# Kernel tuning notes

Hardware: AMD Instinct MI355X
Metric: run time of the kernel (lower is better)

## Reference

```python
import jax, jax.numpy as jnp
import numpy as np


def _prelu(x, a):
    # torch.nn.PReLU with per-channel parameter a (broadcast over batch)
    return jnp.where(x >= 0, x, a * x)


def setup_inputs() -> dict:
    key = jax.random.key(0)
    ks = jax.random.split(key, 12)
    B = 8192
    dims = [512, 1024, 1024, 512]  # tardim
    E = 8                          # tctrl = modim[-1]
    scale = 0.02                   # keep activations well-scaled across 3 layers
    inp = {
        "x": jax.random.normal(ks[0], (B, dims[0]), dtype=jnp.float32),
        "weights": jax.random.uniform(ks[1], (E,), dtype=jnp.float32),
    }
    for i in range(3):
        din, dout = dims[i], dims[i + 1]
        inp[f"W{i}"] = jax.random.normal(ks[2 + 3 * i], (E, din, dout), dtype=jnp.float32) * scale
        inp[f"b{i}"] = jax.random.normal(ks[3 + 3 * i], (E, dout), dtype=jnp.float32) * scale
        inp[f"a{i}"] = jnp.full((dout,), 0.25, dtype=jnp.float32)  # PReLU init
    return inp


def reference(x, weights, W0, b0, a0, W1, b1, a1, W2, b2, a2):
    # mie.g: per layer, weighted sum over tctrl expert Linears, then PReLU.
    # sum_j (w_j/sum(w)) * (x @ W_j + b_j) == x @ (sum_j wn_j W_j) + sum_j wn_j b_j,
    # so pre-merge expert weights (tiny contraction) and do one GEMM per layer.
    wn = weights / jnp.sum(weights)  # [E]
    for W, b, a in ((W0, b0, a0), (W1, b1, a1), (W2, b2, a2)):
        Wm = jnp.einsum('e,eio->io', wn, W)  # merged weight [in, out]
        bm = jnp.einsum('e,eo->o', wn, b)    # merged bias   [out]
        x = _prelu(x @ Wm + bm, a)           # [B, out]
    return x
```

## Files before the change

kernel.cpp:

```cpp
#include <hip/hip_runtime.h>
#include <stdint.h>

typedef unsigned short u16;
typedef __attribute__((ext_vector_type(8))) short short8;
typedef __attribute__((ext_vector_type(4))) float float4v;

__device__ __forceinline__ u16 f2bf(float f) {
    union { float f; uint32_t u; } v; v.f = f;
    uint32_t r = v.u + 0x7fffu + ((v.u >> 16) & 1u);
    return (u16)(r >> 16);
}

__device__ __forceinline__ void gload16(const u16* g, u16* l) {
    __builtin_amdgcn_global_load_lds(
        (const __attribute__((address_space(1))) void*)g,
        (__attribute__((address_space(3))) void*)l, 16, 0, 0);
}

__device__ __forceinline__ float load_wn(const float* wts, float* wn) {
    float s = 0.f;
    #pragma unroll
    for (int e = 0; e < 8; ++e) { wn[e] = wts[e]; s += wn[e]; }
    return 1.0f / s;
}

__device__ __forceinline__ void merge_tile(
    const float* __restrict__ W, u16* __restrict__ Wt, int K, int N, int lb,
    const float* wn, float inv, float (*tile)[33], int tid) {
    const int ntiles = N >> 5;
    const int o0 = (lb % ntiles) * 32, i0 = (lb / ntiles) * 32;
    const int tx = tid & 31, ty = tid >> 5;
    #pragma unroll
    for (int s4 = 0; s4 < 4; ++s4) {
        int il = ty + s4 * 8;
        float acc = 0.f;
        #pragma unroll
        for (int e = 0; e < 8; ++e)
            acc += wn[e] * W[(size_t)e * K * N + (size_t)(i0 + il) * N + o0 + tx];
        tile[il][tx] = acc * inv;
    }
    __syncthreads();
    #pragma unroll
    for (int s4 = 0; s4 < 4; ++s4) {
        int ol = ty + s4 * 8;
        Wt[(size_t)(o0 + ol) * K + i0 + tx] = f2bf(tile[tx][ol]);
    }
}

__global__ __launch_bounds__(256) void prep_fused(
    const float* __restrict__ x, u16* __restrict__ xbf,
    const float* __restrict__ wts,
    const float* __restrict__ W0, u16* __restrict__ W0t,
    const float* __restrict__ b0, const float* __restrict__ b1, const float* __restrict__ b2,
    float* __restrict__ bm) {
    __shared__ float tile[32][33];
    const int b = blockIdx.x, tid = threadIdx.x;

    if (b < 4096) {
        int i = (b * 256 + tid) * 4;
        float4 v = *(const float4*)(x + i);
        union { u16 s[4]; uint64_t q; } o;
        o.s[0] = f2bf(v.x); o.s[1] = f2bf(v.y); o.s[2] = f2bf(v.z); o.s[3] = f2bf(v.w);
        *(uint64_t*)(xbf + i) = o.q;
        return;
    }

    float wn[8]; const float inv = load_wn(wts, wn);

    if (b < 4608) {
        merge_tile(W0, W0t, 512, 1024, b - 4096, wn, inv, tile, tid);
        return;
    }

    int t = (b - 4608) * 256 + tid;
    if (t >= 2560) return;
    const float* bp; int o, stride;
    if (t < 1024)      { bp = b0; o = t;        stride = 1024; }
    else if (t < 2048) { bp = b1; o = t - 1024; stride = 1024; }
    else               { bp = b2; o = t - 2048; stride = 512;  }
    float acc = 0.f;
    #pragma unroll
    for (int e = 0; e < 8; ++e) acc += wn[e] * bp[e * stride + o];
    bm[t] = acc * inv;
}

template <int BN, bool OUT_F32, bool MERGE>
__global__ __launch_bounds__(256, 2) void gemm_bias_prelu(
    const u16* __restrict__ A, const u16* __restrict__ Bt,
    const float* __restrict__ bias, const float* __restrict__ alpha,
    void* __restrict__ outp, int M, int N, int K,
    const float* __restrict__ wts, const float* __restrict__ Wm,
    u16* __restrict__ Wmt, int K2, int N2) {
    __shared__ __align__(16) u16 sh[(128 + BN) * 64];
    const int tid = threadIdx.x;
    const int nbn = N / BN;
    const int nGemm = nbn * (M >> 7);
    const int bid = blockIdx.x;

    if (MERGE && bid >= nGemm) {
        float wn[8]; const float inv = load_wn(wts, wn);
        merge_tile(Wm, Wmt, K2, N2, bid - nGemm, wn, inv, (float(*)[33])(void*)sh, tid);
        return;
    }

    const int bn = bid % nbn, bm = bid / nbn;
    u16* As = sh;
    u16* Bs = sh + 128 * 64;

    const int r0 = tid >> 3;
    const int p  = tid & 7;
    const int c  = p ^ (r0 & 7);
    const u16* Ag = A  + (size_t)(bm * 128 + r0) * K + c * 8;
    const u16* Bg = Bt + (size_t)(bn * BN  + r0) * K + c * 8;
    u16* Al = As + tid * 8;
    u16* Bl = Bs + tid * 8;

    const int lane = tid & 63, w = tid >> 6;
    constexpr int WN = BN / 2;
    constexpr int NI = WN / 16;
    const int wm = (w >> 1) * 64, wncol = (w & 1) * WN;
    const int l16 = lane & 15, quad = lane >> 4;
    const int xr = l16 & 7;
    const short8* As8 = (const short8*)As;
    const short8* Bs8 = (const short8*)Bs;

    float4v acc[4][NI] = {};

    const int nk = K >> 6;
    for (int kt = 0; kt < nk; ++kt) {
        #pragma unroll
        for (int it = 0; it < 4; ++it)
            gload16(Ag + (size_t)(it * 32) * K, Al + it * 2048);
        #pragma unroll
        for (int it = 0; it < BN / 32; ++it)
            gload16(Bg + (size_t)(it * 32) * K, Bl + it * 2048);
        __syncthreads();
        #pragma unroll
        for (int kk = 0; kk < 2; ++kk) {
            const int cb = kk * 4;
            short8 af[4], bf[NI];
            #pragma unroll
            for (int mi = 0; mi < 4; ++mi)
                af[mi] = As8[(wm + mi * 16 + l16) * 8 + ((cb + quad) ^ xr)];
            #pragma unroll
            for (int ni = 0; ni < NI; ++ni)
                bf[ni] = Bs8[(wncol + ni * 16 + l16) * 8 + ((cb + quad) ^ xr)];
            #pragma unroll
            for (int mi = 0; mi < 4; ++mi)
                #pragma unroll
                for (int ni = 0; ni < NI; ++ni)
                    acc[mi][ni] = __builtin_amdgcn_mfma_f32_16x16x32_bf16(
                        af[mi], bf[ni], acc[mi][ni], 0, 0, 0);
        }
        if (kt + 1 < nk) __syncthreads();
        Ag += 64; Bg += 64;
    }

    const int cbase = bn * BN + wncol + l16;
    float bv[NI], av[NI];
    #pragma unroll
    for (int ni = 0; ni < NI; ++ni) { bv[ni] = bias[cbase + ni * 16]; av[ni] = alpha[cbase + ni * 16]; }
    const int rbase = bm * 128 + wm + quad * 4;
    #pragma unroll
    for (int mi = 0; mi < 4; ++mi) {
        #pragma unroll
        for (int reg = 0; reg < 4; ++reg) {
            int r = rbase + mi * 16 + reg;
            #pragma unroll
            for (int ni = 0; ni < NI; ++ni) {
                float v = acc[mi][ni][reg] + bv[ni];
                v = v >= 0.f ? v : av[ni] * v;
                size_t idx = (size_t)r * N + cbase + ni * 16;
                if (OUT_F32) ((float*)outp)[idx] = v;
                else         ((u16*)outp)[idx] = f2bf(v);
            }
        }
    }
}

extern "C" void kernel_launch(void* const* d_in, const int* in_sizes, int n_in,
                              void* d_out, int out_size, void* d_ws, size_t ws_size,
                              hipStream_t stream) {
    const float* x   = (const float*)d_in[0];
    const float* wts = (const float*)d_in[1];
    const float* W0  = (const float*)d_in[2];
    const float* b0  = (const float*)d_in[3];
    const float* a0  = (const float*)d_in[4];
    const float* W1  = (const float*)d_in[5];
    const float* b1  = (const float*)d_in[6];
    const float* a1  = (const float*)d_in[7];
    const float* W2  = (const float*)d_in[8];
    const float* b2  = (const float*)d_in[9];
    const float* a2  = (const float*)d_in[10];
    float* out = (float*)d_out;

    char* ws = (char*)d_ws;
    u16*   xbf  = (u16*)ws;  ws += (size_t)8192 * 512 * 2;
    u16*   act1 = (u16*)ws;  ws += (size_t)8192 * 1024 * 2;
    u16*   act2 = (u16*)ws;  ws += (size_t)8192 * 1024 * 2;
    u16*   W0t  = (u16*)ws;  ws += (size_t)1024 * 512 * 2;
    u16*   W1t  = (u16*)ws;  ws += (size_t)1024 * 1024 * 2;
    u16*   W2t  = (u16*)ws;  ws += (size_t)512 * 1024 * 2;
    float* bm   = (float*)ws;

    prep_fused<<<4618, 256, 0, stream>>>(x, xbf, wts, W0, W0t, b0, b1, b2, bm);

    gemm_bias_prelu<128, false, true><<<512 + 1024, 256, 0, stream>>>(
        xbf, W0t, bm, a0, act1, 8192, 1024, 512,
        wts, W1, W1t, 1024, 1024);

    gemm_bias_prelu<128, false, true><<<512 + 512, 256, 0, stream>>>(
        act1, W1t, bm + 1024, a1, act2, 8192, 1024, 1024,
        wts, W2, W2t, 1024, 512);

    gemm_bias_prelu<64, true, false><<<512, 256, 0, stream>>>(
        act2, W2t, bm + 2048, a2, out, 8192, 512, 1024,
        nullptr, nullptr, nullptr, 0, 0);
}
```

Before: 197.2 us.

## Double-buffer LDS tiles in GEMM to overlap global loads with MFMA

Doubles the shared-memory staging buffer in the bias+PReLU GEMM and prefetches the next K-tile into the alternate buffer while the current tile feeds the MFMAs. This leaves one barrier per K-step instead of two. The aim is to hide global-to-LDS load latency behind compute. The cost is twice the LDS per block, which could limit occupancy. The overlap may also be lost if the compiler waits on the outstanding direct-to-LDS loads before the LDS reads.

Result: slower. 201.7 us (+2.3%).

```diff
diff --git a/kernel.cpp b/kernel.cpp
--- a/kernel.cpp
+++ b/kernel.cpp
@@ -91,7 +91,8 @@
     void* __restrict__ outp, int M, int N, int K,
     const float* __restrict__ wts, const float* __restrict__ Wm,
     u16* __restrict__ Wmt, int K2, int N2) {
-    __shared__ __align__(16) u16 sh[(128 + BN) * 64];
+    constexpr int BUFE = (128 + BN) * 64;
+    __shared__ __align__(16) u16 sh[2 * BUFE];
     const int tid = threadIdx.x;
     const int nbn = N / BN;
     const int nGemm = nbn * (M >> 7);
@@ -104,16 +105,12 @@
     }
 
     const int bn = bid % nbn, bm = bid / nbn;
-    u16* As = sh;
-    u16* Bs = sh + 128 * 64;
 
     const int r0 = tid >> 3;
     const int p  = tid & 7;
     const int c  = p ^ (r0 & 7);
     const u16* Ag = A  + (size_t)(bm * 128 + r0) * K + c * 8;
     const u16* Bg = Bt + (size_t)(bn * BN  + r0) * K + c * 8;
-    u16* Al = As + tid * 8;
-    u16* Bl = Bs + tid * 8;
 
     const int lane = tid & 63, w = tid >> 6;
     constexpr int WN = BN / 2;
@@ -121,30 +118,50 @@
     const int wm = (w >> 1) * 64, wncol = (w & 1) * WN;
     const int l16 = lane & 15, quad = lane >> 4;
     const int xr = l16 & 7;
-    const short8* As8 = (const short8*)As;
-    const short8* Bs8 = (const short8*)Bs;
 
     float4v acc[4][NI] = {};
-
     const int nk = K >> 6;
-    for (int kt = 0; kt < nk; ++kt) {
+
+    {
+        u16* Al = sh + tid * 8;
+        u16* Bl = sh + 128 * 64 + tid * 8;
         #pragma unroll
         for (int it = 0; it < 4; ++it)
             gload16(Ag + (size_t)(it * 32) * K, Al + it * 2048);
         #pragma unroll
         for (int it = 0; it < BN / 32; ++it)
             gload16(Bg + (size_t)(it * 32) * K, Bl + it * 2048);
+    }
+    Ag += 64; Bg += 64;
+
+    int cur = 0;
+    for (int kt = 0; kt < nk; ++kt) {
         __syncthreads();
+
+        if (kt + 1 < nk) {
+            u16* Al = sh + (cur ^ 1) * BUFE + tid * 8;
+            u16* Bl = sh + (cur ^ 1) * BUFE + 128 * 64 + tid * 8;
+            #pragma unroll
+            for (int it = 0; it < 4; ++it)
+                gload16(Ag + (size_t)(it * 32) * K, Al + it * 2048);
+            #pragma unroll
+            for (int it = 0; it < BN / 32; ++it)
+                gload16(Bg + (size_t)(it * 32) * K, Bl + it * 2048);
+            Ag += 64; Bg += 64;
+        }
+
+        const short8* A8 = (const short8*)(sh + cur * BUFE);
+        const short8* B8 = (const short8*)(sh + cur * BUFE + 128 * 64);
         #pragma unroll
         for (int kk = 0; kk < 2; ++kk) {
             const int cb = kk * 4;
             short8 af[4], bf[NI];
             #pragma unroll
             for (int mi = 0; mi < 4; ++mi)
-                af[mi] = As8[(wm + mi * 16 + l16) * 8 + ((cb + quad) ^ xr)];
+                af[mi] = A8[(wm + mi * 16 + l16) * 8 + ((cb + quad) ^ xr)];
             #pragma unroll
             for (int ni = 0; ni < NI; ++ni)
-                bf[ni] = Bs8[(wncol + ni * 16 + l16) * 8 + ((cb + quad) ^ xr)];
+                bf[ni] = B8[(wncol + ni * 16 + l16) * 8 + ((cb + quad) ^ xr)];
             #pragma unroll
             for (int mi = 0; mi < 4; ++mi)
                 #pragma unroll
@@ -152,8 +169,7 @@
                     acc[mi][ni] = __builtin_amdgcn_mfma_f32_16x16x32_bf16(
                         af[mi], bf[ni], acc[mi][ni], 0, 0, 0);
         }
-        if (kt + 1 < nk) __syncthreads();
-        Ag += 64; Bg += 64;
+        cur ^= 1;
     }
 
     const int cbase = bn * BN + wncol + l16;
```
